# Performance work log

Hardware: AMD Instinct MI355X
Metric: run time of the kernel (lower is better)

Reference implementation:

```python
import jax, jax.numpy as jnp
import numpy as np

B_SZ, L, D_MODEL = 2, 1024, 1024
EXPAND, D_STATE, D_CONV = 2, 16, 4
D_INNER = D_MODEL * EXPAND
DT_RANK = max(D_MODEL // 16, 1)


def setup_inputs() -> dict:
    key = jax.random.key(0)
    ks = jax.random.split(key, 9)
    s = 0.02
    x = jax.random.normal(ks[0], (B_SZ, L, D_MODEL), jnp.float32)
    W_in = jax.random.normal(ks[1], (2 * D_INNER, D_MODEL), jnp.float32) * s
    conv_w = jax.random.normal(ks[2], (D_INNER, D_CONV), jnp.float32) * 0.1
    conv_b = jax.random.normal(ks[3], (D_INNER,), jnp.float32) * 0.01
    W_x = jax.random.normal(ks[4], (DT_RANK + 2 * D_STATE, D_INNER), jnp.float32) * s
    W_dt = jax.random.normal(ks[5], (D_INNER, DT_RANK), jnp.float32) * s
    b_dt = jax.random.normal(ks[6], (D_INNER,), jnp.float32) * 0.01
    A_log = jnp.log(jnp.broadcast_to(jnp.arange(1, D_STATE + 1, dtype=jnp.float32), (D_INNER, D_STATE)))
    D_param = jnp.ones((D_INNER,), jnp.float32)
    W_out = jax.random.normal(ks[7], (D_MODEL, D_INNER), jnp.float32) * s
    return {"x": x, "W_in": W_in, "conv_w": conv_w, "conv_b": conv_b,
            "W_x": W_x, "W_dt": W_dt, "b_dt": b_dt, "A_log": A_log,
            "D_param": D_param, "W_out": W_out}


def _mamba_fwd(x, W_in, conv_w, conv_b, W_x, W_dt, b_dt, A_log, D_param, W_out):
    # in-proj and gate split
    xz = jnp.einsum("bld,ed->ble", x, W_in)            # (B, L, 2*d_inner)
    x_ssm, z = jnp.split(xz, 2, axis=-1)
    # causal depthwise 1D conv (left pad d_conv-1 == torch pad-both + [:L])
    xc = x_ssm.transpose(0, 2, 1)                        # (B, d_inner, L)
    xc = jax.lax.conv_general_dilated(
        xc, conv_w[:, None, :], window_strides=(1,),
        padding=[(D_CONV - 1, 0)], feature_group_count=D_INNER,
        dimension_numbers=("NCH", "OIH", "NCH"))
    xc = xc + conv_b[None, :, None]
    x_ssm = jax.nn.silu(xc.transpose(0, 2, 1))           # (B, L, d_inner)
    # input-dependent dt, B, C
    dbc = jnp.einsum("bld,ed->ble", x_ssm, W_x)
    dt, B_sel, C_sel = jnp.split(dbc, [DT_RANK, DT_RANK + D_STATE], axis=-1)
    delta = jax.nn.softplus(jnp.einsum("blr,dr->bld", dt, W_dt) + b_dt)
    A = -jnp.exp(A_log)                                  # (d_inner, d_state)
    # discretization
    deltaA = jnp.exp(delta[..., None] * A)               # (B, L, d_inner, d_state)
    dBu = delta[..., None] * B_sel[:, :, None, :] * x_ssm[..., None]
    # linear recurrence h_t = deltaA_t * h_{t-1} + dBu_t via associative scan
    def comb(e1, e2):
        a1, b1 = e1
        a2, b2 = e2
        return (a1 * a2, a2 * b1 + b2)
    _, h = jax.lax.associative_scan(comb, (deltaA, dBu), axis=1)
    y = jnp.sum(h * C_sel[:, :, None, :], axis=-1)       # (B, L, d_inner)
    y = y + x_ssm * D_param
    y = y * jax.nn.silu(z)
    return jnp.einsum("ble,de->bld", y, W_out)


def reference(x, W_in, conv_w, conv_b, W_x, W_dt, b_dt, A_log, D_param, W_out):
    return _mamba_fwd(x, W_in, conv_w, conv_b, W_x, W_dt, b_dt, A_log, D_param, W_out)
```

## Files before the change

### kernel.cpp

```cpp
#include <hip/hip_runtime.h>
#include <hip/hip_bf16.h>

#define B_SZ   2
#define SEQ    1024
#define DMODEL 1024
#define DINNER 2048
#define DSTATE 16
#define DCONV  4
#define DTRANK 64
#define BLROWS (B_SZ*SEQ)
#define NCHUNK 16
#define TCHUNK (SEQ/NCHUNK)

using floatx4 = __attribute__((ext_vector_type(4))) float;
using short8  = __attribute__((ext_vector_type(8))) short;
using us8     = __attribute__((ext_vector_type(8))) unsigned short;
using us4     = __attribute__((ext_vector_type(4))) unsigned short;

__device__ __forceinline__ float softplus_f(float x) {
    return fmaxf(x, 0.f) + log1pf(__expf(-fabsf(x)));
}
__device__ __forceinline__ float silu_f(float x) {
    return x / (1.f + __expf(-x));
}
__device__ __forceinline__ short bfs(float x) {
    union { __hip_bfloat16 h; short s; } u;
    u.h = __float2bfloat16(x);
    return u.s;
}
__device__ __forceinline__ float b2f(unsigned short s) {
    union { float f; unsigned u; } x;
    x.u = ((unsigned)s) << 16;
    return x.f;
}
__device__ __forceinline__ void gld16(const void* g, void* l) {
    __builtin_amdgcn_global_load_lds((const __attribute__((address_space(1))) void*)g,
                                     (__attribute__((address_space(3))) void*)l,
                                     16, 0, 0);
}
__device__ __forceinline__ void cast8(const float* src, unsigned short* dst, int i) {
    const float* p = src + (size_t)i*8;
    float4 a = *(const float4*)p, b = *(const float4*)(p+4);
    us8 o;
    o[0]=(unsigned short)bfs(a.x); o[1]=(unsigned short)bfs(a.y);
    o[2]=(unsigned short)bfs(a.z); o[3]=(unsigned short)bfs(a.w);
    o[4]=(unsigned short)bfs(b.x); o[5]=(unsigned short)bfs(b.y);
    o[6]=(unsigned short)bfs(b.z); o[7]=(unsigned short)bfs(b.w);
    *(us8*)(dst + (size_t)i*8) = o;
}

#define G0 (BLROWS*DMODEL/8)
#define G1 (2*DINNER*DMODEL/8)
#define G2 (96*DINNER/8)
#define G3 (DINNER*DTRANK/8)
#define G4 (DMODEL*DINNER/8)
#define G5 (BLROWS*DMODEL/8)
#define G6 (BLROWS*96/8)
#define GTOT (G0+G1+G2+G3+G4+G5+G6)
__global__ __launch_bounds__(256)
void init_kernel(const float* __restrict__ x, const float* __restrict__ W_in,
                 const float* __restrict__ W_x, const float* __restrict__ W_dt,
                 const float* __restrict__ W_out,
                 unsigned short* xH, unsigned short* WinH, unsigned short* WxH,
                 unsigned short* WdtH, unsigned short* WoutH,
                 float* outZ, float* dbcZ)
{
    int i = blockIdx.x*256 + threadIdx.x;
    if (i < G0) { cast8(x, xH, i); return; }            i -= G0;
    if (i < G1) { cast8(W_in, WinH, i); return; }       i -= G1;
    if (i < G2) { cast8(W_x, WxH, i); return; }         i -= G2;
    if (i < G3) { cast8(W_dt, WdtH, i); return; }       i -= G3;
    if (i < G4) { cast8(W_out, WoutH, i); return; }     i -= G4;
    if (i < G5) {
        float4 z = {0,0,0,0};
        *(float4*)(outZ + (size_t)i*8) = z; *(float4*)(outZ + (size_t)i*8 + 4) = z;
        return;
    }                                                    i -= G5;
    if (i < G6) {
        float4 z = {0,0,0,0};
        *(float4*)(dbcZ + (size_t)i*8) = z; *(float4*)(dbcZ + (size_t)i*8 + 4) = z;
    }
}

template<int TN, int EPI, bool NGUARD>
__global__ __launch_bounds__(256)
void gemm_tn(const __hip_bfloat16* __restrict__ Ag, const __hip_bfloat16* __restrict__ Bg,
             int M, int N, int K, int kslice,
             float* __restrict__ outF,
             __hip_bfloat16* __restrict__ outH,
             __hip_bfloat16* __restrict__ outH2,
             const float* __restrict__ bias)
{
    constexpr int EB  = TN/64;
    constexpr int FNW = TN/32;
    __shared__ short As[128*32];
    __shared__ short Bs[TN*32];

    const int tid  = threadIdx.x;
    const int lane = tid & 63, wave = tid >> 6;
    const int bm0  = blockIdx.x * 128;
    const int bn0  = blockIdx.y * TN;
    const int kbeg = blockIdx.z * kslice;
    const int kend = kbeg + kslice;
    const int wrow = (wave >> 1) * 64, wcol = (wave & 1) * (TN/2);
    const int lrow = lane & 15, quad = lane >> 4;

    const int srow = wave*16 + (lane >> 2);
    const int scol = (lane & 3) * 8;

    const __hip_bfloat16* ga0 = Ag + (size_t)(bm0 + srow)*K      + scol;
    const __hip_bfloat16* ga1 = Ag + (size_t)(bm0 + srow + 64)*K + scol;
    const __hip_bfloat16* gb0 = Bg + (size_t)(bn0 + srow)*K      + scol;
    const __hip_bfloat16* gb1 = (EB > 1) ? Bg + (size_t)(bn0 + srow + 64)*K + scol : nullptr;
    short* lA0 = &As[(wave*16)*32];      short* lA1 = &As[(wave*16 + 64)*32];
    short* lB0 = &Bs[(wave*16)*32];
    short* lB1 = (EB > 1) ? &Bs[(wave*16 + 64)*32] : nullptr;
    const bool b0ok = !NGUARD || (bn0 + wave*16) < N;
    const bool b1ok = (EB > 1) && (!NGUARD || (bn0 + wave*16 + 64) < N);

    floatx4 acc[4][FNW] = {};

    for (int k0 = kbeg; k0 < kend; k0 += 32) {
        gld16(ga0 + k0, lA0);
        gld16(ga1 + k0, lA1);
        if (b0ok) gld16(gb0 + k0, lB0);
        if (EB > 1 && b1ok) gld16(gb1 + k0, lB1);
        __syncthreads();

        short8 af[4], bf[FNW];
        #pragma unroll
        for (int i = 0; i < 4; i++)
            af[i] = *(const short8*)&As[(wrow + i*16 + lrow)*32 + quad*8];
        #pragma unroll
        for (int j = 0; j < FNW; j++)
            bf[j] = *(const short8*)&Bs[(wcol + j*16 + lrow)*32 + quad*8];
        #pragma unroll
        for (int i = 0; i < 4; i++)
            #pragma unroll
            for (int j = 0; j < FNW; j++)
                acc[i][j] = __builtin_amdgcn_mfma_f32_16x16x32_bf16(af[i], bf[j], acc[i][j], 0, 0, 0);
        __syncthreads();
    }

    const int rq = quad * 4;
    #pragma unroll
    for (int i = 0; i < 4; i++) {
        #pragma unroll
        for (int j = 0; j < FNW; j++) {
            int col = bn0 + wcol + j*16 + lrow;
            if (NGUARD && col >= N) continue;
            if constexpr (EPI == 8) {
                int row0 = bm0 + wrow + i*16 + rq;
                int bb = row0 >> 10, ll = row0 & (SEQ-1);
                us4 pk;
                #pragma unroll
                for (int r = 0; r < 4; r++)
                    pk[r] = (unsigned short)bfs(softplus_f(acc[i][j][r] + bias[col]));
                *(us4*)((unsigned short*)outH + ((size_t)bb*DINNER + col)*SEQ + ll) = pk;
            } else {
                #pragma unroll
                for (int r = 0; r < 4; r++) {
                    int row = bm0 + wrow + i*16 + rq + r;
                    float v = acc[i][j][r];
                    if constexpr (EPI == 5) {
                        if (col < DINNER)
                            outH[(size_t)row*DINNER + col] = __float2bfloat16(v);
                        else
                            outH2[(size_t)row*DINNER + (col - DINNER)] = __float2bfloat16(v);
                    } else if constexpr (EPI == 7) {
                        atomicAdd(&outF[(size_t)row*N + col], v);
                    }
                }
            }
        }
    }
}

__global__ __launch_bounds__(256)
void dt_cvt_kernel(const float* __restrict__ dbc, __hip_bfloat16* __restrict__ dtH) {
    int i = blockIdx.x*256 + threadIdx.x;
    int row = i >> 6, col = i & 63;
    dtH[i] = __float2bfloat16(dbc[(size_t)row*96 + col]);
}

__global__ __launch_bounds__(256)
void conv_transpose_kernel(const unsigned short* __restrict__ xbufN,
                           const float* __restrict__ cw,
                           const float* __restrict__ cb,
                           unsigned short* __restrict__ xsN,
                           unsigned short* __restrict__ xsT)
{
    __shared__ unsigned short t[67*68];
    __shared__ unsigned short t2[64*68];
    const int tid = threadIdx.x;
    const int l0 = blockIdx.x * 64, d0 = blockIdx.y * 64, b = blockIdx.z;

    const int lc4 = (tid & 15) * 4;
    for (int r = tid >> 4; r < 67; r += 16) {
        int lg = l0 - 3 + r;
        us4 v = {0,0,0,0};
        if (lg >= 0)
            v = *(const us4*)&xbufN[((size_t)(b*SEQ + lg))*DINNER + d0 + lc4];
        *(us4*)&t[r*68 + lc4] = v;
    }
    __syncthreads();

    const int dd = tid & 63;
    float4 w4 = *(const float4*)&cw[(d0 + dd)*4];
    float  bb = cb[d0 + dd];
    #pragma unroll 4
    for (int rr = tid >> 6; rr < 64; rr += 4) {
        float acc = bb;
        acc += w4.x * b2f(t[(rr+0)*68 + dd]);
        acc += w4.y * b2f(t[(rr+1)*68 + dd]);
        acc += w4.z * b2f(t[(rr+2)*68 + dd]);
        acc += w4.w * b2f(t[(rr+3)*68 + dd]);
        unsigned short h = (unsigned short)bfs(silu_f(acc));
        t2[rr*68 + dd] = h;
        xsN[((size_t)(b*SEQ + l0 + rr))*DINNER + d0 + dd] = h;
    }
    __syncthreads();

    const int dr = tid >> 4, lc = tid & 15;
    #pragma unroll
    for (int i = 0; i < 4; i++) {
        int dT = dr + i*16;
        us4 w;
        #pragma unroll
        for (int j = 0; j < 4; j++)
            w[j] = t2[(lc*4 + j)*68 + dT];
        *(us4*)&xsT[((size_t)b*DINNER + d0 + dT)*SEQ + l0 + lc*4] = w;
    }
}

__global__ __launch_bounds__(256)
void scan_pass1(const unsigned short* __restrict__ deT,
                const unsigned short* __restrict__ xsT,
                const float* __restrict__ dbc,
                const float* __restrict__ A_log,
                float* __restrict__ Bc, float* __restrict__ sde)
{
    const int tid  = threadIdx.x;
    const int q    = tid & 3, dsub = tid >> 2;
    const int blk  = blockIdx.x;
    const int dg   = blk & 31;
    const int c    = (blk >> 5) & 15;
    const int b    = blk >> 9;
    const int d    = dg*64 + dsub;

    float An[4];
    *(float4*)An = *(const float4*)&A_log[d*DSTATE + 4*q];
    #pragma unroll
    for (int j = 0; j < 4; j++) An[j] = -__expf(An[j]);

    size_t rowT = ((size_t)b*DINNER + d)*SEQ;
    size_t b96  = (size_t)b*SEQ*96;

    float h[4] = {0.f,0.f,0.f,0.f};
    float s = 0.f;
    for (int t8 = 0; t8 < TCHUNK/8; ++t8) {
        int l0 = c*TCHUNK + t8*8;
        us8 de8 = *(const us8*)&deT[rowT + l0];
        us8 u8  = *(const us8*)&xsT[rowT + l0];
        #pragma unroll
        for (int j2 = 0; j2 < 8; j2++) {
            int l = l0 + j2;
            float Bn[4];
            *(float4*)Bn = *(const float4*)&dbc[b96 + (size_t)l*96 + DTRANK + 4*q];
            float de = b2f(de8[j2]);
            float du = de * b2f(u8[j2]);
            #pragma unroll
            for (int j = 0; j < 4; j++)
                h[j] = __expf(de*An[j])*h[j] + du*Bn[j];
            s += de;
        }
    }
    size_t ci = (size_t)(b*NCHUNK + c)*DINNER + d;
    *(float4*)&Bc[ci*16 + 4*q] = *(float4*)h;
    if (q == 0) sde[ci] = s;
}

__global__ __launch_bounds__(256)
void scan_pass2(float* __restrict__ Bc, const float* __restrict__ sde,
                const float* __restrict__ A_log)
{
    const int tid = threadIdx.x;
    const int n   = tid & 15, dl = tid >> 4;
    const int blk = blockIdx.x;
    const int dg  = blk & 127, b = blk >> 7;
    const int d   = dg*16 + dl;
    const float An = -__expf(A_log[d*DSTATE + n]);

    float H = 0.f;
    for (int c = 0; c < NCHUNK; ++c) {
        size_t ci = (size_t)(b*NCHUNK + c)*DINNER + d;
        float bc = Bc[ci*16 + n];
        Bc[ci*16 + n] = H;
        H = __expf(An*sde[ci])*H + bc;
    }
}

__global__ __launch_bounds__(256)
void scan_pass3(const unsigned short* __restrict__ deT,
                const unsigned short* __restrict__ xsT,
                const float* __restrict__ dbc,
                const float* __restrict__ A_log,
                const float* __restrict__ Dp,
                const float* __restrict__ Hinit,
                __hip_bfloat16* __restrict__ yN)
{
    const int tid  = threadIdx.x;
    const int q    = tid & 3, dsub = tid >> 2;
    const int blk  = blockIdx.x;
    const int dg   = blk & 31;
    const int c    = (blk >> 5) & 15;
    const int b    = blk >> 9;
    const int d    = dg*64 + dsub;

    float An[4];
    *(float4*)An = *(const float4*)&A_log[d*DSTATE + 4*q];
    #pragma unroll
    for (int j = 0; j < 4; j++) An[j] = -__expf(An[j]);
    const float Dd = Dp[d];

    size_t rowT  = ((size_t)b*DINNER + d)*SEQ;
    size_t baseN = (size_t)b*SEQ*DINNER + d;
    size_t b96   = (size_t)b*SEQ*96;

    float h[4];
    *(float4*)h = *(const float4*)&Hinit[((size_t)(b*NCHUNK + c)*DINNER + d)*16 + 4*q];

    for (int t8 = 0; t8 < TCHUNK/8; ++t8) {
        int l0 = c*TCHUNK + t8*8;
        us8 de8 = *(const us8*)&deT[rowT + l0];
        us8 u8  = *(const us8*)&xsT[rowT + l0];
        #pragma unroll
        for (int j2 = 0; j2 < 8; j2++) {
            int l = l0 + j2;
            float Bn[4], Cn[4];
            *(float4*)Bn = *(const float4*)&dbc[b96 + (size_t)l*96 + DTRANK + 4*q];
            *(float4*)Cn = *(const float4*)&dbc[b96 + (size_t)l*96 + DTRANK + DSTATE + 4*q];
            float de = b2f(de8[j2]);
            float u  = b2f(u8[j2]);
            float du = de * u;
            float cc = 0.f;
            #pragma unroll
            for (int j = 0; j < 4; j++) {
                h[j] = __expf(de*An[j])*h[j] + du*Bn[j];
                cc += h[j]*Cn[j];
            }
            cc += __shfl_xor(cc, 1);
            cc += __shfl_xor(cc, 2);
            if (q == 0)
                yN[baseN + (size_t)l*DINNER] = __float2bfloat16(cc + u*Dd);
        }
    }
}

__global__ __launch_bounds__(256)
void gate_kernel(unsigned short* __restrict__ y, const unsigned short* __restrict__ z) {
    size_t i = ((size_t)blockIdx.x*256 + threadIdx.x) * 4;
    us4 yv = *(const us4*)&y[i];
    us4 zv = *(const us4*)&z[i];
    us4 o;
    #pragma unroll
    for (int j = 0; j < 4; j++)
        o[j] = (unsigned short)bfs(b2f(yv[j]) * silu_f(b2f(zv[j])));
    *(us4*)&y[i] = o;
}

__global__ __launch_bounds__(256)
void zero_out_kernel(float* out, int n) {
    int i = blockIdx.x * 256 + threadIdx.x;
    if (i < n) out[i] = 0.f;
}

extern "C" void kernel_launch(void* const* d_in, const int* in_sizes, int n_in,
                              void* d_out, int out_size, void* d_ws, size_t ws_size,
                              hipStream_t stream) {
    const float* x      = (const float*)d_in[0];
    const float* W_in   = (const float*)d_in[1];
    const float* conv_w = (const float*)d_in[2];
    const float* conv_b = (const float*)d_in[3];
    const float* W_x    = (const float*)d_in[4];
    const float* W_dt   = (const float*)d_in[5];
    const float* b_dt   = (const float*)d_in[6];
    const float* A_log  = (const float*)d_in[7];
    const float* D_par  = (const float*)d_in[8];
    const float* W_out  = (const float*)d_in[9];

    size_t szBig = (size_t)BLROWS * DINNER * 2;
    size_t szBc  = (size_t)B_SZ * NCHUNK * DINNER * DSTATE * 4;
    size_t need  = 5*szBig
                 + (size_t)BLROWS*96*4 + (size_t)BLROWS*DTRANK*2
                 + szBc + (size_t)B_SZ*NCHUNK*DINNER*4
                 + (size_t)BLROWS*DMODEL*2
                 + (size_t)2*DINNER*DMODEL*2
                 + (size_t)128*DINNER*2
                 + (size_t)DINNER*DTRANK*2
                 + (size_t)DMODEL*DINNER*2;

    if (ws_size < need) {
        zero_out_kernel<<<(out_size + 255)/256, 256, 0, stream>>>((float*)d_out, out_size);
        return;
    }

    char* w = (char*)d_ws;
    __hip_bfloat16* xbufN = (__hip_bfloat16*)w;  w += szBig;
    __hip_bfloat16* zbufN = (__hip_bfloat16*)w;  w += szBig;
    __hip_bfloat16* xsN   = (__hip_bfloat16*)w;  w += szBig;
    __hip_bfloat16* xsT   = (__hip_bfloat16*)w;  w += szBig;
    __hip_bfloat16* deT   = (__hip_bfloat16*)w;  w += szBig;
    float*          dbc   = (float*)w;           w += (size_t)BLROWS * 96 * 4;
    __hip_bfloat16* dtH   = (__hip_bfloat16*)w;  w += (size_t)BLROWS * DTRANK * 2;
    float*          Bc    = (float*)w;           w += szBc;
    float*          sde   = (float*)w;           w += (size_t)B_SZ * NCHUNK * DINNER * 4;
    __hip_bfloat16* xH    = (__hip_bfloat16*)w;  w += (size_t)BLROWS*DMODEL*2;
    __hip_bfloat16* WinH  = (__hip_bfloat16*)w;  w += (size_t)2*DINNER*DMODEL*2;
    __hip_bfloat16* WxH   = (__hip_bfloat16*)w;  w += (size_t)128*DINNER*2;
    __hip_bfloat16* WdtH  = (__hip_bfloat16*)w;  w += (size_t)DINNER*DTRANK*2;
    __hip_bfloat16* WoutH = (__hip_bfloat16*)w;  w += (size_t)DMODEL*DINNER*2;
    __hip_bfloat16* yN    = xsN;

    init_kernel<<<GTOT/256, 256, 0, stream>>>(x, W_in, W_x, W_dt, W_out,
        (unsigned short*)xH, (unsigned short*)WinH, (unsigned short*)WxH,
        (unsigned short*)WdtH, (unsigned short*)WoutH, (float*)d_out, dbc);

    gemm_tn<64,5,false><<<dim3(BLROWS/128, (2*DINNER)/64, 1), 256, 0, stream>>>(
        xH, WinH, BLROWS, 2*DINNER, DMODEL, DMODEL, nullptr, xbufN, zbufN, nullptr);

    conv_transpose_kernel<<<dim3(SEQ/64, DINNER/64, B_SZ), 256, 0, stream>>>(
        (const unsigned short*)xbufN, conv_w, conv_b,
        (unsigned short*)xsN, (unsigned short*)xsT);

    gemm_tn<64,7,true><<<dim3(BLROWS/128, 2, 16), 256, 0, stream>>>(
        xsN, WxH, BLROWS, 96, DINNER, DINNER/16, dbc, nullptr, nullptr, nullptr);
    dt_cvt_kernel<<<(BLROWS*DTRANK)/256, 256, 0, stream>>>(dbc, dtH);

    gemm_tn<64,8,false><<<dim3(BLROWS/128, DINNER/64, 1), 256, 0, stream>>>(
        dtH, WdtH, BLROWS, DINNER, DTRANK, DTRANK, nullptr, deT, nullptr, b_dt);

    scan_pass1<<<B_SZ*NCHUNK*32, 256, 0, stream>>>((const unsigned short*)deT,
        (const unsigned short*)xsT, dbc, A_log, Bc, sde);
    scan_pass2<<<B_SZ*128, 256, 0, stream>>>(Bc, sde, A_log);
    scan_pass3<<<B_SZ*NCHUNK*32, 256, 0, stream>>>((const unsigned short*)deT,
        (const unsigned short*)xsT, dbc, A_log, D_par, Bc, yN);

    gate_kernel<<<(BLROWS*DINNER)/(256*4), 256, 0, stream>>>(
        (unsigned short*)yN, (const unsigned short*)zbufN);

    gemm_tn<64,7,false><<<dim3(BLROWS/128, DMODEL/64, 4), 256, 0, stream>>>(
        yN, WoutH, BLROWS, DMODEL, DINNER, DINNER/4, (float*)d_out, nullptr, nullptr, nullptr);
}
```

Baseline: 259.3 us.

## Double-buffer GEMM LDS, replace atomics with split-K partials, fuse gate into scan

The shared GEMM kernel now double-buffers its LDS tiles so the next K-slice loads are issued while the current slice is multiplied. The x-projection GEMM writes per-slice partial sums that a new reduce kernel adds up, and that kernel also emits the bf16 dt matrix; this replaces the float atomicAdds and the separate dt conversion. The output GEMM runs without split-K and stores directly, so the zeroing of out and dbc in init is dropped. The SiLU(z) gating moves into scan_pass3's store, removing the standalone gate kernel, and the in-projection uses 128-wide N tiles. In exchange there is an extra partial buffer, twice the LDS per block, and a no-split-K output GEMM with only 256 blocks.

```diff
diff --git a/kernel.cpp b/kernel.cpp
--- a/kernel.cpp
+++ b/kernel.cpp
@@ -11,6 +11,7 @@
 #define BLROWS (B_SZ*SEQ)
 #define NCHUNK 16
 #define TCHUNK (SEQ/NCHUNK)
+#define NSLICE 16
 
 using floatx4 = __attribute__((ext_vector_type(4))) float;
 using short8  = __attribute__((ext_vector_type(8))) short;
@@ -54,32 +55,20 @@
 #define G2 (96*DINNER/8)
 #define G3 (DINNER*DTRANK/8)
 #define G4 (DMODEL*DINNER/8)
-#define G5 (BLROWS*DMODEL/8)
-#define G6 (BLROWS*96/8)
-#define GTOT (G0+G1+G2+G3+G4+G5+G6)
+#define GTOT (G0+G1+G2+G3+G4)
 __global__ __launch_bounds__(256)
 void init_kernel(const float* __restrict__ x, const float* __restrict__ W_in,
                  const float* __restrict__ W_x, const float* __restrict__ W_dt,
                  const float* __restrict__ W_out,
                  unsigned short* xH, unsigned short* WinH, unsigned short* WxH,
-                 unsigned short* WdtH, unsigned short* WoutH,
-                 float* outZ, float* dbcZ)
+                 unsigned short* WdtH, unsigned short* WoutH)
 {
     int i = blockIdx.x*256 + threadIdx.x;
     if (i < G0) { cast8(x, xH, i); return; }            i -= G0;
     if (i < G1) { cast8(W_in, WinH, i); return; }       i -= G1;
     if (i < G2) { cast8(W_x, WxH, i); return; }         i -= G2;
     if (i < G3) { cast8(W_dt, WdtH, i); return; }       i -= G3;
-    if (i < G4) { cast8(W_out, WoutH, i); return; }     i -= G4;
-    if (i < G5) {
-        float4 z = {0,0,0,0};
-        *(float4*)(outZ + (size_t)i*8) = z; *(float4*)(outZ + (size_t)i*8 + 4) = z;
-        return;
-    }                                                    i -= G5;
-    if (i < G6) {
-        float4 z = {0,0,0,0};
-        *(float4*)(dbcZ + (size_t)i*8) = z; *(float4*)(dbcZ + (size_t)i*8 + 4) = z;
-    }
+    if (i < G4) { cast8(W_out, WoutH, i); }
 }
 
 template<int TN, int EPI, bool NGUARD>
@@ -93,8 +82,8 @@
 {
     constexpr int EB  = TN/64;
     constexpr int FNW = TN/32;
-    __shared__ short As[128*32];
-    __shared__ short Bs[TN*32];
+    __shared__ short As[2][128*32];
+    __shared__ short Bs[2][TN*32];
 
     const int tid  = threadIdx.x;
     const int lane = tid & 63, wave = tid >> 6;
@@ -112,34 +101,37 @@
     const __hip_bfloat16* ga1 = Ag + (size_t)(bm0 + srow + 64)*K + scol;
     const __hip_bfloat16* gb0 = Bg + (size_t)(bn0 + srow)*K      + scol;
     const __hip_bfloat16* gb1 = (EB > 1) ? Bg + (size_t)(bn0 + srow + 64)*K + scol : nullptr;
-    short* lA0 = &As[(wave*16)*32];      short* lA1 = &As[(wave*16 + 64)*32];
-    short* lB0 = &Bs[(wave*16)*32];
-    short* lB1 = (EB > 1) ? &Bs[(wave*16 + 64)*32] : nullptr;
     const bool b0ok = !NGUARD || (bn0 + wave*16) < N;
     const bool b1ok = (EB > 1) && (!NGUARD || (bn0 + wave*16 + 64) < N);
 
+    auto stage = [&](int c, int k0) {
+        gld16(ga0 + k0, &As[c][(wave*16)*32]);
+        gld16(ga1 + k0, &As[c][(wave*16 + 64)*32]);
+        if (b0ok) gld16(gb0 + k0, &Bs[c][(wave*16)*32]);
+        if (EB > 1 && b1ok) gld16(gb1 + k0, &Bs[c][(wave*16 + 64)*32]);
+    };
+
     floatx4 acc[4][FNW] = {};
 
+    stage(0, kbeg);
+    __syncthreads();
+    int cur = 0;
     for (int k0 = kbeg; k0 < kend; k0 += 32) {
-        gld16(ga0 + k0, lA0);
-        gld16(ga1 + k0, lA1);
-        if (b0ok) gld16(gb0 + k0, lB0);
-        if (EB > 1 && b1ok) gld16(gb1 + k0, lB1);
-        __syncthreads();
-
+        if (k0 + 32 < kend) stage(cur ^ 1, k0 + 32);
         short8 af[4], bf[FNW];
         #pragma unroll
         for (int i = 0; i < 4; i++)
-            af[i] = *(const short8*)&As[(wrow + i*16 + lrow)*32 + quad*8];
+            af[i] = *(const short8*)&As[cur][(wrow + i*16 + lrow)*32 + quad*8];
         #pragma unroll
         for (int j = 0; j < FNW; j++)
-            bf[j] = *(const short8*)&Bs[(wcol + j*16 + lrow)*32 + quad*8];
+            bf[j] = *(const short8*)&Bs[cur][(wcol + j*16 + lrow)*32 + quad*8];
         #pragma unroll
         for (int i = 0; i < 4; i++)
             #pragma unroll
             for (int j = 0; j < FNW; j++)
                 acc[i][j] = __builtin_amdgcn_mfma_f32_16x16x32_bf16(af[i], bf[j], acc[i][j], 0, 0, 0);
         __syncthreads();
+        cur ^= 1;
     }
 
     const int rq = quad * 4;
@@ -167,8 +159,8 @@
                             outH[(size_t)row*DINNER + col] = __float2bfloat16(v);
                         else
                             outH2[(size_t)row*DINNER + (col - DINNER)] = __float2bfloat16(v);
-                    } else if constexpr (EPI == 7) {
-                        atomicAdd(&outF[(size_t)row*N + col], v);
+                    } else if constexpr (EPI == 9) {
+                        outF[(size_t)blockIdx.z*M*N + (size_t)row*N + col] = v;
                     }
                 }
             }
@@ -176,11 +168,22 @@
     }
 }
 
-__global__ __launch_bounds__(256)
-void dt_cvt_kernel(const float* __restrict__ dbc, __hip_bfloat16* __restrict__ dtH) {
-    int i = blockIdx.x*256 + threadIdx.x;
-    int row = i >> 6, col = i & 63;
-    dtH[i] = __float2bfloat16(dbc[(size_t)row*96 + col]);
+__global__ __launch_bounds__(192)
+void dbc_reduce_kernel(const float* __restrict__ part, float* __restrict__ dbc,
+                       __hip_bfloat16* __restrict__ dtH)
+{
+    const int tid = threadIdx.x;
+    const int r2  = (tid >= 96) ? 1 : 0;
+    const int col = tid - 96*r2;
+    const int row = blockIdx.x*2 + r2;
+    const size_t idx = (size_t)row*96 + col;
+    float s = 0.f;
+    #pragma unroll
+    for (int z = 0; z < NSLICE; z++)
+        s += part[(size_t)z*(BLROWS*96) + idx];
+    dbc[idx] = s;
+    if (col < DTRANK)
+        dtH[(size_t)row*DTRANK + col] = __float2bfloat16(s);
 }
 
 __global__ __launch_bounds__(256)
@@ -307,6 +310,7 @@
                 const float* __restrict__ A_log,
                 const float* __restrict__ Dp,
                 const float* __restrict__ Hinit,
+                const unsigned short* __restrict__ zN,
                 __hip_bfloat16* __restrict__ yN)
 {
     const int tid  = threadIdx.x;
@@ -351,22 +355,12 @@
             }
             cc += __shfl_xor(cc, 1);
             cc += __shfl_xor(cc, 2);
-            if (q == 0)
-                yN[baseN + (size_t)l*DINNER] = __float2bfloat16(cc + u*Dd);
+            if (q == 0) {
+                float zv = silu_f(b2f(zN[baseN + (size_t)l*DINNER]));
+                yN[baseN + (size_t)l*DINNER] = __float2bfloat16((cc + u*Dd) * zv);
+            }
         }
     }
-}
-
-__global__ __launch_bounds__(256)
-void gate_kernel(unsigned short* __restrict__ y, const unsigned short* __restrict__ z) {
-    size_t i = ((size_t)blockIdx.x*256 + threadIdx.x) * 4;
-    us4 yv = *(const us4*)&y[i];
-    us4 zv = *(const us4*)&z[i];
-    us4 o;
-    #pragma unroll
-    for (int j = 0; j < 4; j++)
-        o[j] = (unsigned short)bfs(b2f(yv[j]) * silu_f(b2f(zv[j])));
-    *(us4*)&y[i] = o;
 }
 
 __global__ __launch_bounds__(256)
@@ -392,7 +386,9 @@
     size_t szBig = (size_t)BLROWS * DINNER * 2;
     size_t szBc  = (size_t)B_SZ * NCHUNK * DINNER * DSTATE * 4;
     size_t need  = 5*szBig
-                 + (size_t)BLROWS*96*4 + (size_t)BLROWS*DTRANK*2
+                 + (size_t)BLROWS*96*4
+                 + (size_t)NSLICE*BLROWS*96*4
+                 + (size_t)BLROWS*DTRANK*2
                  + szBc + (size_t)B_SZ*NCHUNK*DINNER*4
                  + (size_t)BLROWS*DMODEL*2
                  + (size_t)2*DINNER*DMODEL*2
@@ -412,6 +408,7 @@
     __hip_bfloat16* xsT   = (__hip_bfloat16*)w;  w += szBig;
     __hip_bfloat16* deT   = (__hip_bfloat16*)w;  w += szBig;
     float*          dbc   = (float*)w;           w += (size_t)BLROWS * 96 * 4;
+    float*          dbcP  = (float*)w;           w += (size_t)NSLICE * BLROWS * 96 * 4;
     __hip_bfloat16* dtH   = (__hip_bfloat16*)w;  w += (size_t)BLROWS * DTRANK * 2;
     float*          Bc    = (float*)w;           w += szBc;
     float*          sde   = (float*)w;           w += (size_t)B_SZ * NCHUNK * DINNER * 4;
@@ -424,18 +421,18 @@
 
     init_kernel<<<GTOT/256, 256, 0, stream>>>(x, W_in, W_x, W_dt, W_out,
         (unsigned short*)xH, (unsigned short*)WinH, (unsigned short*)WxH,
-        (unsigned short*)WdtH, (unsigned short*)WoutH, (float*)d_out, dbc);
-
-    gemm_tn<64,5,false><<<dim3(BLROWS/128, (2*DINNER)/64, 1), 256, 0, stream>>>(
+        (unsigned short*)WdtH, (unsigned short*)WoutH);
+
+    gemm_tn<128,5,false><<<dim3(BLROWS/128, (2*DINNER)/128, 1), 256, 0, stream>>>(
         xH, WinH, BLROWS, 2*DINNER, DMODEL, DMODEL, nullptr, xbufN, zbufN, nullptr);
 
     conv_transpose_kernel<<<dim3(SEQ/64, DINNER/64, B_SZ), 256, 0, stream>>>(
         (const unsigned short*)xbufN, conv_w, conv_b,
         (unsigned short*)xsN, (unsigned short*)xsT);
 
-    gemm_tn<64,7,true><<<dim3(BLROWS/128, 2, 16), 256, 0, stream>>>(
-        xsN, WxH, BLROWS, 96, DINNER, DINNER/16, dbc, nullptr, nullptr, nullptr);
-    dt_cvt_kernel<<<(BLROWS*DTRANK)/256, 256, 0, stream>>>(dbc, dtH);
+    gemm_tn<64,9,true><<<dim3(BLROWS/128, 2, NSLICE), 256, 0, stream>>>(
+        xsN, WxH, BLROWS, 96, DINNER, DINNER/NSLICE, dbcP, nullptr, nullptr, nullptr);
+    dbc_reduce_kernel<<<BLROWS/2, 192, 0, stream>>>(dbcP, dbc, dtH);
 
     gemm_tn<64,8,false><<<dim3(BLROWS/128, DINNER/64, 1), 256, 0, stream>>>(
         dtH, WdtH, BLROWS, DINNER, DTRANK, DTRANK, nullptr, deT, nullptr, b_dt);
@@ -444,11 +441,9 @@
         (const unsigned short*)xsT, dbc, A_log, Bc, sde);
     scan_pass2<<<B_SZ*128, 256, 0, stream>>>(Bc, sde, A_log);
     scan_pass3<<<B_SZ*NCHUNK*32, 256, 0, stream>>>((const unsigned short*)deT,
-        (const unsigned short*)xsT, dbc, A_log, D_par, Bc, yN);
-
-    gate_kernel<<<(BLROWS*DINNER)/(256*4), 256, 0, stream>>>(
-        (unsigned short*)yN, (const unsigned short*)zbufN);
-
-    gemm_tn<64,7,false><<<dim3(BLROWS/128, DMODEL/64, 4), 256, 0, stream>>>(
-        yN, WoutH, BLROWS, DMODEL, DINNER, DINNER/4, (float*)d_out, nullptr, nullptr, nullptr);
-}
+        (const unsigned short*)xsT, dbc, A_log, D_par, Bc,
+        (const unsigned short*)zbufN, yN);
+
+    gemm_tn<64,9,false><<<dim3(BLROWS/128, DMODEL/64, 1), 256, 0, stream>>>(
+        yN, WoutH, BLROWS, DMODEL, DINNER, DINNER, (float*)d_out, nullptr, nullptr, nullptr);
+}
```

After: 258.9 us. No clear change (-0.1%).
